# Performance work log

Measured on AMD Instinct MI355X. Metric: run time of the kernel, lower is better.

The kernel has to match this reference:

```python
import jax, jax.numpy as jnp
import numpy as np

N = 100000      # nodes
E = 1600000     # edges
F_IN = 64       # num_features
H = 64          # nhid
G = 512         # num graphs in batch
C = 2           # num_classes
BN_EPS = 1e-5


def setup_inputs() -> dict:
    key = jax.random.key(0)
    ks = jax.random.split(key, 8)
    x = jax.random.normal(ks[0], (N, F_IN), jnp.float32)
    edge_index = jax.random.randint(ks[1], (2, E), 0, N, dtype=jnp.int64)
    batch = jnp.sort(jax.random.randint(ks[2], (N,), 0, G, dtype=jnp.int64))
    s = lambda k, shp, fan: (jax.random.normal(k, shp, jnp.float32) / np.sqrt(fan)).astype(jnp.float32)
    W1 = s(ks[3], (F_IN, H), F_IN); b1 = jnp.zeros((H,), jnp.float32)
    W2 = s(ks[4], (H, H), H);       b2 = jnp.zeros((H,), jnp.float32)
    Wg = s(ks[5], (H, 1), H);       bg = jnp.zeros((1,), jnp.float32)
    bn_gamma = jnp.ones((H,), jnp.float32); bn_beta = jnp.zeros((H,), jnp.float32)
    bn_mean = jnp.zeros((H,), jnp.float32); bn_var = jnp.ones((H,), jnp.float32)
    W_lin = s(ks[6], (H, C), H);    b_lin = jnp.zeros((C,), jnp.float32)
    return dict(x=x, edge_index=edge_index, batch=batch,
                W1=W1, b1=b1, W2=W2, b2=b2, Wg=Wg, bg=bg,
                bn_gamma=bn_gamma, bn_beta=bn_beta, bn_mean=bn_mean, bn_var=bn_var,
                W_lin=W_lin, b_lin=b_lin)


def reference(x, edge_index, batch, W1, b1, W2, b2, Wg, bg,
              bn_gamma, bn_beta, bn_mean, bn_var, W_lin, b_lin):
    src, dst = edge_index[0], edge_index[1]
    # GINConv (eps=0): h_i = MLP(x_i + sum_{j->i} x_j)
    agg = jax.ops.segment_sum(x[src], dst, num_segments=N)       # [N, F_IN]
    h = x + agg
    h = jnp.maximum(h @ W1 + b1, 0.0) @ W2 + b2                  # [N, H]
    h = jnp.maximum(h, 0.0)                                      # outer ReLU
    # Attentional aggregation: segment softmax of gate, weighted segment-sum
    gate = (h @ Wg + bg)[:, 0]                                   # [N]
    gmax = jax.ops.segment_max(gate, batch, num_segments=G)      # [G]
    ex = jnp.exp(gate - gmax[batch])                             # [N]
    denom = jax.ops.segment_sum(ex, batch, num_segments=G)       # [G]
    alpha = ex / denom[batch]                                    # [N]
    pooled = jax.ops.segment_sum(alpha[:, None] * h, batch, num_segments=G)  # [G, H]
    # BatchNorm1d in eval mode (running stats); dropout is identity in eval
    norm = (pooled - bn_mean) / jnp.sqrt(bn_var + BN_EPS) * bn_gamma + bn_beta
    logits = norm @ W_lin + b_lin                                # [G, C]
    return jax.nn.log_softmax(logits, axis=-1)
```

## Files before the change

kernel.cpp:

```cpp
#include <hip/hip_runtime.h>
#include <math.h>
#include <float.h>

#define BN_EPS 1e-5f
#define PBLK   8192
#define NBUCKP 832
#define ACAP   4096
#define STCAP  3072

typedef short s16x8 __attribute__((ext_vector_type(8)));
typedef float f32x4 __attribute__((ext_vector_type(4)));

__device__ __forceinline__ unsigned short f2bf(float f) {
    unsigned u = __float_as_uint(f);
    u += 0x7FFFu + ((u >> 16) & 1u);
    return (unsigned short)(u >> 16);
}
__device__ __forceinline__ float bf2f(unsigned short b) {
    return __uint_as_float(((unsigned)b) << 16);
}

__global__ __launch_bounds__(512) void prep_partition(
    const float* __restrict__ x, unsigned short* __restrict__ xb,
    const float* __restrict__ W1, const float* __restrict__ W2,
    unsigned short* __restrict__ w1t, unsigned short* __restrict__ w2t,
    const int* __restrict__ src, const int* __restrict__ dst,
    int* __restrict__ bcur0, int* __restrict__ packed2,
    int N, int E, int EB)
{
    __shared__ int hist[NBUCKP], lstart[NBUCKP], goff[NBUCKP], cur[NBUCKP];
    __shared__ int sorted[PBLK];
    __shared__ unsigned short sbkt[PBLK];

    int tid = threadIdx.x;
    int lane = tid & 63;
    int blk = blockIdx.x;

    int n4 = N * 16;
    for (int i = blk * 512 + tid; i < n4; i += gridDim.x * 512) {
        float4 f = *(const float4*)(x + (size_t)i * 4);
        ushort4 o;
        o.x = f2bf(f.x); o.y = f2bf(f.y); o.z = f2bf(f.z); o.w = f2bf(f.w);
        *(ushort4*)(xb + (size_t)i * 4) = o;
    }
    if (blk == 0)
        for (int idx = tid; idx < 4096; idx += 512)
            w1t[idx] = f2bf(W1[(idx & 63) * 64 + (idx >> 6)]);
    if (blk == 1)
        for (int idx = tid; idx < 4096; idx += 512)
            w2t[idx] = f2bf(W2[(idx & 63) * 64 + (idx >> 6)]);

    if (blk >= EB) return;

    int e0 = blk * PBLK;
    int cnt = E - e0; if (cnt > PBLK) cnt = PBLK; if (cnt < 0) cnt = 0;

    for (int i = tid; i < NBUCKP; i += 512) hist[i] = 0;
    __syncthreads();
    for (int i = tid; i < cnt; i += 512)
        atomicAdd(&hist[dst[e0 + i] >> 7], 1);
    __syncthreads();
    if (tid < 64) {
        int carry = 0;
        #pragma unroll
        for (int c = 0; c < NBUCKP / 64; ++c) {
            int idx = c * 64 + lane;
            int v = hist[idx];
            int xv = v;
            #pragma unroll
            for (int d = 1; d < 64; d <<= 1) {
                int t = __shfl_up(xv, d); if (lane >= d) xv += t;
            }
            lstart[idx] = xv - v + carry;
            carry += __shfl(xv, 63);
        }
    }
    __syncthreads();
    for (int i = tid; i < NBUCKP; i += 512) {
        cur[i] = lstart[i];
        if (hist[i] > 0) goff[i] = atomicAdd(&bcur0[i], hist[i]);
    }
    __syncthreads();
    for (int i = tid; i < cnt; i += 512) {
        int d = dst[e0 + i];
        int s = src[e0 + i];
        int b = d >> 7;
        int p = atomicAdd(&cur[b], 1);
        sorted[p] = ((d & 127) << 17) | s;
        sbkt[p] = (unsigned short)b;
    }
    __syncthreads();
    for (int i = tid; i < cnt; i += 512) {
        int b = sbkt[i];
        packed2[(size_t)b * ACAP + goff[b] + (i - lstart[b])] = sorted[i];
    }
}

__global__ __launch_bounds__(512) void bucket_fused(
    const unsigned short* __restrict__ xb,
    const int* __restrict__ packed2, const int* __restrict__ bcur0,
    const unsigned short* __restrict__ w1t, const unsigned short* __restrict__ w2t,
    const float* __restrict__ b1, const float* __restrict__ b2,
    const float* __restrict__ Wg, const float* __restrict__ bg,
    unsigned short* __restrict__ h_out, float* __restrict__ gate_out, int N)
{
    __shared__ int hist[128], excl[129], cur[128];
    __shared__ int stage[STCAP];
    __shared__ unsigned short vt[128][72];

    int tid = threadIdx.x;
    int lane = tid & 63;
    int wave = tid >> 6;
    int b = blockIdx.x;
    int node0 = b * 128;
    int ecnt = bcur0[b];
    if (ecnt > ACAP) ecnt = ACAP;
    const int* arena = packed2 + (size_t)b * ACAP;

    if (tid < 128) hist[tid] = 0;
    __syncthreads();
    for (int i = tid; i < ecnt; i += 512)
        atomicAdd(&hist[arena[i] >> 17], 1);
    __syncthreads();
    if (tid < 64) {
        int carry = 0;
        #pragma unroll
        for (int c = 0; c < 2; ++c) {
            int idx = c * 64 + lane;
            int v = hist[idx];
            int xv = v;
            #pragma unroll
            for (int d = 1; d < 64; d <<= 1) {
                int t = __shfl_up(xv, d); if (lane >= d) xv += t;
            }
            excl[idx] = xv - v + carry;
            carry += __shfl(xv, 63);
        }
        if (lane == 0) excl[128] = carry;
    }
    __syncthreads();
    if (tid < 128) cur[tid] = excl[tid];
    __syncthreads();
    for (int i = tid; i < ecnt; i += 512) {
        int v = arena[i];
        int p = atomicAdd(&cur[v >> 17], 1);
        if (p < STCAP) stage[p] = v & 0x1FFFF;
    }
    __syncthreads();

    int rowbase = wave * 16;
    for (int m = 0; m < 16; ++m) {
        int ln = rowbase + m;
        int node = node0 + ln;
        if (node < N) {
            int beg = excl[ln];     if (beg > STCAP) beg = STCAP;
            int end = excl[ln + 1]; if (end > STCAP) end = STCAP;

            float v0 = bf2f(xb[(size_t)node * 64 + lane]);
            float v1 = 0.f, v2 = 0.f, v3 = 0.f, v4 = 0.f, v5 = 0.f, v6 = 0.f, v7 = 0.f;

            for (int base = beg; base < end; base += 64) {
                int ei = (base + lane < end) ? stage[base + lane] : 0;
                int cnt = end - base; if (cnt > 64) cnt = 64;
                int j = 0;
                for (; j + 8 <= cnt; j += 8) {
                    int s0 = __builtin_amdgcn_readlane(ei, j + 0);
                    int s1 = __builtin_amdgcn_readlane(ei, j + 1);
                    int s2 = __builtin_amdgcn_readlane(ei, j + 2);
                    int s3 = __builtin_amdgcn_readlane(ei, j + 3);
                    int s4 = __builtin_amdgcn_readlane(ei, j + 4);
                    int s5 = __builtin_amdgcn_readlane(ei, j + 5);
                    int s6 = __builtin_amdgcn_readlane(ei, j + 6);
                    int s7 = __builtin_amdgcn_readlane(ei, j + 7);
                    unsigned short t0 = xb[(size_t)s0 * 64 + lane];
                    unsigned short t1 = xb[(size_t)s1 * 64 + lane];
                    unsigned short t2 = xb[(size_t)s2 * 64 + lane];
                    unsigned short t3 = xb[(size_t)s3 * 64 + lane];
                    unsigned short t4 = xb[(size_t)s4 * 64 + lane];
                    unsigned short t5 = xb[(size_t)s5 * 64 + lane];
                    unsigned short t6 = xb[(size_t)s6 * 64 + lane];
                    unsigned short t7 = xb[(size_t)s7 * 64 + lane];
                    v0 += bf2f(t0); v1 += bf2f(t1); v2 += bf2f(t2); v3 += bf2f(t3);
                    v4 += bf2f(t4); v5 += bf2f(t5); v6 += bf2f(t6); v7 += bf2f(t7);
                }
                for (; j + 4 <= cnt; j += 4) {
                    int s0 = __builtin_amdgcn_readlane(ei, j + 0);
                    int s1 = __builtin_amdgcn_readlane(ei, j + 1);
                    int s2 = __builtin_amdgcn_readlane(ei, j + 2);
                    int s3 = __builtin_amdgcn_readlane(ei, j + 3);
                    unsigned short t0 = xb[(size_t)s0 * 64 + lane];
                    unsigned short t1 = xb[(size_t)s1 * 64 + lane];
                    unsigned short t2 = xb[(size_t)s2 * 64 + lane];
                    unsigned short t3 = xb[(size_t)s3 * 64 + lane];
                    v4 += bf2f(t0); v5 += bf2f(t1); v6 += bf2f(t2); v7 += bf2f(t3);
                }
                for (; j < cnt; ++j) {
                    int s = __builtin_amdgcn_readlane(ei, j);
                    v1 += bf2f(xb[(size_t)s * 64 + lane]);
                }
            }
            float v = ((v0 + v1) + (v2 + v3)) + ((v4 + v5) + (v6 + v7));
            vt[ln][lane] = f2bf(v);
        } else {
            vt[ln][lane] = 0;
        }
    }

    {
        int quad = lane >> 4;
        int col  = lane & 15;

        s16x8 a0 = *(const s16x8*)&vt[rowbase + col][quad * 8];
        s16x8 a1 = *(const s16x8*)&vt[rowbase + col][32 + quad * 8];

        float b1v[4], b2v[4], wgv[4];
        #pragma unroll
        for (int nt = 0; nt < 4; ++nt) {
            b1v[nt] = b1[nt * 16 + col];
            b2v[nt] = b2[nt * 16 + col];
            wgv[nt] = Wg[nt * 16 + col];
        }
        float bgv = bg[0];

        f32x4 acc1[4];
        #pragma unroll
        for (int nt = 0; nt < 4; ++nt) {
            int off = (nt * 16 + col) * 64 + quad * 8;
            s16x8 w0 = *(const s16x8*)(w1t + off);
            s16x8 w1 = *(const s16x8*)(w1t + off + 32);
            f32x4 c = {0.f, 0.f, 0.f, 0.f};
            c = __builtin_amdgcn_mfma_f32_16x16x32_bf16(a0, w0, c, 0, 0, 0);
            c = __builtin_amdgcn_mfma_f32_16x16x32_bf16(a1, w1, c, 0, 0, 0);
            acc1[nt] = c;
        }
        #pragma unroll
        for (int nt = 0; nt < 4; ++nt)
            #pragma unroll
            for (int r = 0; r < 4; ++r) {
                float hv = fmaxf(acc1[nt][r] + b1v[nt], 0.f);
                vt[rowbase + quad * 4 + r][nt * 16 + col] = f2bf(hv);
            }

        s16x8 g0 = *(const s16x8*)&vt[rowbase + col][quad * 8];
        s16x8 g1 = *(const s16x8*)&vt[rowbase + col][32 + quad * 8];

        f32x4 acc2[4];
        #pragma unroll
        for (int nt = 0; nt < 4; ++nt) {
            int off = (nt * 16 + col) * 64 + quad * 8;
            s16x8 w0 = *(const s16x8*)(w2t + off);
            s16x8 w1 = *(const s16x8*)(w2t + off + 32);
            f32x4 c = {0.f, 0.f, 0.f, 0.f};
            c = __builtin_amdgcn_mfma_f32_16x16x32_bf16(g0, w0, c, 0, 0, 0);
            c = __builtin_amdgcn_mfma_f32_16x16x32_bf16(g1, w1, c, 0, 0, 0);
            acc2[nt] = c;
        }

        int nbase = node0 + rowbase;
        float gp[4] = {0.f, 0.f, 0.f, 0.f};
        #pragma unroll
        for (int nt = 0; nt < 4; ++nt)
            #pragma unroll
            for (int r = 0; r < 4; ++r) {
                float hv = fmaxf(acc2[nt][r] + b2v[nt], 0.f);
                int node = nbase + quad * 4 + r;
                if (node < N)
                    h_out[(size_t)node * 64 + nt * 16 + col] = f2bf(hv);
                gp[r] = fmaf(hv, wgv[nt], gp[r]);
            }
        #pragma unroll
        for (int r = 0; r < 4; ++r) {
            float t = gp[r];
            t += __shfl_xor(t, 1);
            t += __shfl_xor(t, 2);
            t += __shfl_xor(t, 4);
            t += __shfl_xor(t, 8);
            int node = nbase + quad * 4 + r;
            if (col == 0 && node < N) gate_out[node] = t + bgv;
        }
    }
}

__global__ __launch_bounds__(256) void pool_final(
    const unsigned short* __restrict__ h, const float* __restrict__ gate,
    const int* __restrict__ batch,
    const float* __restrict__ gamma_, const float* __restrict__ beta_,
    const float* __restrict__ mean_, const float* __restrict__ var_,
    const float* __restrict__ Wl, const float* __restrict__ bl,
    float* __restrict__ out, int N)
{
    int g = blockIdx.x;
    int tid = threadIdx.x;

    int lo = 0, hi = N;
    while (lo < hi) { int mid = (lo + hi) >> 1; if (batch[mid] < g) lo = mid + 1; else hi = mid; }
    int start = lo;
    hi = N;
    while (lo < hi) { int mid = (lo + hi) >> 1; if (batch[mid] < g + 1) lo = mid + 1; else hi = mid; }
    int end = lo;

    __shared__ float red[4];
    __shared__ float pool_s[4 * 64];

    int lane = tid & 63;
    int wave = tid >> 6;

    float m = -FLT_MAX;
    for (int i = start + tid; i < end; i += 256) m = fmaxf(m, gate[i]);
    #pragma unroll
    for (int off = 32; off; off >>= 1) m = fmaxf(m, __shfl_xor(m, off));
    if (lane == 0) red[wave] = m;
    __syncthreads();
    m = fmaxf(fmaxf(red[0], red[1]), fmaxf(red[2], red[3]));
    __syncthreads();

    float s = 0.f;
    for (int i = start + tid; i < end; i += 256) s += expf(gate[i] - m);
    #pragma unroll
    for (int off = 32; off; off >>= 1) s += __shfl_xor(s, off);
    if (lane == 0) red[wave] = s;
    __syncthreads();
    s = red[0] + red[1] + red[2] + red[3];

    float a0 = 0.f, a1 = 0.f, a2 = 0.f, a3 = 0.f;
    int i = start + wave;
    for (; i + 12 < end; i += 16) {
        float e0 = expf(gate[i]      - m);
        float e1 = expf(gate[i + 4]  - m);
        float e2 = expf(gate[i + 8]  - m);
        float e3 = expf(gate[i + 12] - m);
        float t0 = bf2f(h[(size_t)(i)      * 64 + lane]);
        float t1 = bf2f(h[(size_t)(i + 4)  * 64 + lane]);
        float t2 = bf2f(h[(size_t)(i + 8)  * 64 + lane]);
        float t3 = bf2f(h[(size_t)(i + 12) * 64 + lane]);
        a0 = fmaf(e0, t0, a0);
        a1 = fmaf(e1, t1, a1);
        a2 = fmaf(e2, t2, a2);
        a3 = fmaf(e3, t3, a3);
    }
    for (; i < end; i += 4) {
        float e = expf(gate[i] - m);
        a0 = fmaf(e, bf2f(h[(size_t)i * 64 + lane]), a0);
    }
    pool_s[wave * 64 + lane] = (a0 + a1) + (a2 + a3);
    __syncthreads();

    if (wave == 0) {
        float p = pool_s[lane] + pool_s[64 + lane] + pool_s[128 + lane] + pool_s[192 + lane];
        p = (end > start) ? (p / s) : 0.f;
        float nrm = (p - mean_[lane]) / sqrtf(var_[lane] + BN_EPS) * gamma_[lane] + beta_[lane];
        float l0 = nrm * Wl[lane * 2 + 0];
        float l1 = nrm * Wl[lane * 2 + 1];
        #pragma unroll
        for (int off = 32; off; off >>= 1) {
            l0 += __shfl_xor(l0, off);
            l1 += __shfl_xor(l1, off);
        }
        if (lane == 0) {
            l0 += bl[0];
            l1 += bl[1];
            float mx = fmaxf(l0, l1);
            float lse = mx + logf(expf(l0 - mx) + expf(l1 - mx));
            out[g * 2 + 0] = l0 - lse;
            out[g * 2 + 1] = l1 - lse;
        }
    }
}

extern "C" void kernel_launch(void* const* d_in, const int* in_sizes, int n_in,
                              void* d_out, int out_size, void* d_ws, size_t ws_size,
                              hipStream_t stream)
{
    const float* x     = (const float*)d_in[0];
    const int*   eidx  = (const int*)d_in[1];
    const int*   batch = (const int*)d_in[2];
    const float* W1    = (const float*)d_in[3];
    const float* b1    = (const float*)d_in[4];
    const float* W2    = (const float*)d_in[5];
    const float* b2    = (const float*)d_in[6];
    const float* Wg    = (const float*)d_in[7];
    const float* bg    = (const float*)d_in[8];
    const float* bng   = (const float*)d_in[9];
    const float* bnb   = (const float*)d_in[10];
    const float* bnm   = (const float*)d_in[11];
    const float* bnv   = (const float*)d_in[12];
    const float* Wl    = (const float*)d_in[13];
    const float* bl    = (const float*)d_in[14];
    float* out = (float*)d_out;

    int N = in_sizes[0] / 64;
    int E = in_sizes[1] / 2;
    int G = out_size / 2;
    int NP = ((N + 63) / 64) * 64;
    int NBUCK = (N + 127) / 128;
    int EB = (E + PBLK - 1) / PBLK;
    int GRID_A = 1024 > EB ? 1024 : EB;

    char* w = (char*)d_ws;
    int* packed2 = (int*)w;                     w += (size_t)NBUCK * ACAP * 4;
    unsigned short* hxb  = (unsigned short*)w;  w += (size_t)NP * 64 * 2;
    float* gate  = (float*)w;                   w += ((size_t)N * 4 + 255) / 256 * 256;
    int* bcur0   = (int*)w;                     w += NBUCKP * 4;
    unsigned short* w1t = (unsigned short*)w;   w += 4096 * 2;
    unsigned short* w2t = (unsigned short*)w;   w += 4096 * 2;
    unsigned short* hbuf = (unsigned short*)w;

    const int* src = eidx;
    const int* dst = eidx + E;

    hipMemsetAsync(bcur0, 0, NBUCKP * sizeof(int), stream);

    prep_partition<<<GRID_A, 512, 0, stream>>>(x, hxb, W1, W2, w1t, w2t,
                                               src, dst, bcur0, packed2,
                                               N, E, EB);

    bucket_fused  <<<NBUCK, 512, 0, stream>>>(hxb, packed2, bcur0, w1t, w2t,
                                              b1, b2, Wg, bg, hbuf, gate, N);

    pool_final    <<<G, 256, 0, stream>>>(hbuf, gate, batch, bng, bnb, bnm, bnv,
                                          Wl, bl, out, N);
}
```

Measured before the change: 194.0 us.

## Split node buckets across two smaller blocks and precompute graph segment starts

The fused aggregation+MLP kernel now runs two 256-thread blocks per 128-node bucket, each taking 64 nodes and filtering the shared edge arena by the half bit. This shrinks shared memory per block and doubles the block count, aiming for better occupancy and load spread. The cost is that each block reads the full bucket arena, and the staging capacity per block drops to 2048. Separately, graph segment boundaries are computed once in the prep kernel from adjacent batch ids, replacing the per-block binary searches in pool_final.

```diff
diff --git a/kernel.cpp b/kernel.cpp
--- a/kernel.cpp
+++ b/kernel.cpp
@@ -6,7 +6,7 @@
 #define PBLK   8192
 #define NBUCKP 832
 #define ACAP   4096
-#define STCAP  3072
+#define STCAP  2048
 
 typedef short s16x8 __attribute__((ext_vector_type(8)));
 typedef float f32x4 __attribute__((ext_vector_type(4)));
@@ -25,8 +25,9 @@
     const float* __restrict__ W1, const float* __restrict__ W2,
     unsigned short* __restrict__ w1t, unsigned short* __restrict__ w2t,
     const int* __restrict__ src, const int* __restrict__ dst,
+    const int* __restrict__ batch, int* __restrict__ gstart,
     int* __restrict__ bcur0, int* __restrict__ packed2,
-    int N, int E, int EB)
+    int N, int E, int EB, int G)
 {
     __shared__ int hist[NBUCKP], lstart[NBUCKP], goff[NBUCKP], cur[NBUCKP];
     __shared__ int sorted[PBLK];
@@ -42,6 +43,13 @@
         ushort4 o;
         o.x = f2bf(f.x); o.y = f2bf(f.y); o.z = f2bf(f.z); o.w = f2bf(f.w);
         *(ushort4*)(xb + (size_t)i * 4) = o;
+    }
+    for (int i = blk * 512 + tid; i < N; i += gridDim.x * 512) {
+        int bi = batch[i];
+        int bp = (i == 0) ? -1 : batch[i - 1];
+        for (int g = bp + 1; g <= bi; ++g) gstart[g] = i;
+        if (i == N - 1)
+            for (int g = bi + 1; g <= G; ++g) gstart[g] = N;
     }
     if (blk == 0)
         for (int idx = tid; idx < 4096; idx += 512)
@@ -96,7 +104,7 @@
     }
 }
 
-__global__ __launch_bounds__(512) void bucket_fused(
+__global__ __launch_bounds__(256) void bucket_fused(
     const unsigned short* __restrict__ xb,
     const int* __restrict__ packed2, const int* __restrict__ bcur0,
     const unsigned short* __restrict__ w1t, const unsigned short* __restrict__ w2t,
@@ -104,47 +112,47 @@
     const float* __restrict__ Wg, const float* __restrict__ bg,
     unsigned short* __restrict__ h_out, float* __restrict__ gate_out, int N)
 {
-    __shared__ int hist[128], excl[129], cur[128];
+    __shared__ int hist[64], excl[65], cur[64];
     __shared__ int stage[STCAP];
-    __shared__ unsigned short vt[128][72];
+    __shared__ unsigned short vt[64][72];
 
     int tid = threadIdx.x;
     int lane = tid & 63;
     int wave = tid >> 6;
-    int b = blockIdx.x;
-    int node0 = b * 128;
-    int ecnt = bcur0[b];
+    int bh = blockIdx.x;
+    int bk = bh >> 1;
+    int half = bh & 1;
+    int node0 = bh * 64;
+    int ecnt = bcur0[bk];
     if (ecnt > ACAP) ecnt = ACAP;
-    const int* arena = packed2 + (size_t)b * ACAP;
-
-    if (tid < 128) hist[tid] = 0;
-    __syncthreads();
-    for (int i = tid; i < ecnt; i += 512)
-        atomicAdd(&hist[arena[i] >> 17], 1);
+    const int* arena = packed2 + (size_t)bk * ACAP;
+
+    if (tid < 64) hist[tid] = 0;
+    __syncthreads();
+    for (int i = tid; i < ecnt; i += 256) {
+        int v = arena[i];
+        if ((v >> 23) == half)
+            atomicAdd(&hist[(v >> 17) & 63], 1);
+    }
     __syncthreads();
     if (tid < 64) {
-        int carry = 0;
-        #pragma unroll
-        for (int c = 0; c < 2; ++c) {
-            int idx = c * 64 + lane;
-            int v = hist[idx];
-            int xv = v;
-            #pragma unroll
-            for (int d = 1; d < 64; d <<= 1) {
-                int t = __shfl_up(xv, d); if (lane >= d) xv += t;
-            }
-            excl[idx] = xv - v + carry;
-            carry += __shfl(xv, 63);
-        }
-        if (lane == 0) excl[128] = carry;
-    }
-    __syncthreads();
-    if (tid < 128) cur[tid] = excl[tid];
-    __syncthreads();
-    for (int i = tid; i < ecnt; i += 512) {
+        int v = hist[lane];
+        int xv = v;
+        #pragma unroll
+        for (int d = 1; d < 64; d <<= 1) {
+            int t = __shfl_up(xv, d); if (lane >= d) xv += t;
+        }
+        excl[lane] = xv - v;
+        cur[lane]  = xv - v;
+        if (lane == 63) excl[64] = xv;
+    }
+    __syncthreads();
+    for (int i = tid; i < ecnt; i += 256) {
         int v = arena[i];
-        int p = atomicAdd(&cur[v >> 17], 1);
-        if (p < STCAP) stage[p] = v & 0x1FFFF;
+        if ((v >> 23) == half) {
+            int p = atomicAdd(&cur[(v >> 17) & 63], 1);
+            if (p < STCAP) stage[p] = v & 0x1FFFF;
+        }
     }
     __syncthreads();
 
@@ -283,21 +291,17 @@
 
 __global__ __launch_bounds__(256) void pool_final(
     const unsigned short* __restrict__ h, const float* __restrict__ gate,
-    const int* __restrict__ batch,
+    const int* __restrict__ gstart,
     const float* __restrict__ gamma_, const float* __restrict__ beta_,
     const float* __restrict__ mean_, const float* __restrict__ var_,
     const float* __restrict__ Wl, const float* __restrict__ bl,
-    float* __restrict__ out, int N)
+    float* __restrict__ out)
 {
     int g = blockIdx.x;
     int tid = threadIdx.x;
 
-    int lo = 0, hi = N;
-    while (lo < hi) { int mid = (lo + hi) >> 1; if (batch[mid] < g) lo = mid + 1; else hi = mid; }
-    int start = lo;
-    hi = N;
-    while (lo < hi) { int mid = (lo + hi) >> 1; if (batch[mid] < g + 1) lo = mid + 1; else hi = mid; }
-    int end = lo;
+    int start = gstart[g];
+    int end   = gstart[g + 1];
 
     __shared__ float red[4];
     __shared__ float pool_s[4 * 64];
@@ -393,6 +397,7 @@
     int G = out_size / 2;
     int NP = ((N + 63) / 64) * 64;
     int NBUCK = (N + 127) / 128;
+    int NHALF = (N + 63) / 64;
     int EB = (E + PBLK - 1) / PBLK;
     int GRID_A = 1024 > EB ? 1024 : EB;
 
@@ -403,6 +408,7 @@
     int* bcur0   = (int*)w;                     w += NBUCKP * 4;
     unsigned short* w1t = (unsigned short*)w;   w += 4096 * 2;
     unsigned short* w2t = (unsigned short*)w;   w += 4096 * 2;
+    int* gstart  = (int*)w;                     w += ((size_t)(G + 1) * 4 + 255) / 256 * 256;
     unsigned short* hbuf = (unsigned short*)w;
 
     const int* src = eidx;
@@ -411,12 +417,13 @@
     hipMemsetAsync(bcur0, 0, NBUCKP * sizeof(int), stream);
 
     prep_partition<<<GRID_A, 512, 0, stream>>>(x, hxb, W1, W2, w1t, w2t,
-                                               src, dst, bcur0, packed2,
-                                               N, E, EB);
-
-    bucket_fused  <<<NBUCK, 512, 0, stream>>>(hxb, packed2, bcur0, w1t, w2t,
+                                               src, dst, batch, gstart,
+                                               bcur0, packed2,
+                                               N, E, EB, G);
+
+    bucket_fused  <<<NHALF, 256, 0, stream>>>(hxb, packed2, bcur0, w1t, w2t,
                                               b1, b2, Wg, bg, hbuf, gate, N);
 
-    pool_final    <<<G, 256, 0, stream>>>(hbuf, gate, batch, bng, bnb, bnm, bnv,
-                                          Wl, bl, out, N);
-}
+    pool_final    <<<G, 256, 0, stream>>>(hbuf, gate, gstart, bng, bnb, bnm, bnv,
+                                          Wl, bl, out);
+}
```

Result: slower. 216.0 us (+11.4%).
